# Kernel tuning notes

Measured on AMD Instinct MI355X. Metric: run time of the kernel, lower is better.

Reference implementation:

```python
import jax, jax.numpy as jnp
import numpy as np

N = 50000          # nodes
E = 800000         # edges (avg degree 16)
IN, HID, OUT = 128, 32, 64
H1, H2, H3 = 4, 4, 6
NEG_SLOPE = 0.2


def setup_inputs() -> dict:
    key = jax.random.key(0)
    ks = jax.random.split(key, 18)

    def p(k, shape, fan_in):
        return (jax.random.normal(k, shape, jnp.float32) / np.sqrt(fan_in)).astype(jnp.float32)

    return {
        "x": jax.random.normal(ks[0], (N, IN), jnp.float32),
        "src": jax.random.randint(ks[1], (E,), 0, N, jnp.int32),
        "dst": jax.random.randint(ks[2], (E,), 0, N, jnp.int32),
        # layer 1: IN -> (H1, HID)
        "W1": p(ks[3], (IN, H1 * HID), IN),
        "al1": p(ks[4], (H1, HID), HID),
        "ar1": p(ks[5], (H1, HID), HID),
        "b1": jnp.zeros((H1 * HID,), jnp.float32),
        # layer 2: H1*HID -> (H2, HID), residual (identity since H1*HID == H2*HID... == in)
        "W2": p(ks[6], (H1 * HID, H2 * HID), H1 * HID),
        "al2": p(ks[7], (H2, HID), HID),
        "ar2": p(ks[8], (H2, HID), HID),
        "b2": jnp.zeros((H2 * HID,), jnp.float32),
        # layer 3: H2*HID -> (H3, OUT), residual via linear projection
        "W3": p(ks[9], (H2 * HID, H3 * OUT), H2 * HID),
        "al3": p(ks[10], (H3, OUT), OUT),
        "ar3": p(ks[11], (H3, OUT), OUT),
        "b3": jnp.zeros((H3 * OUT,), jnp.float32),
        "Wres3": p(ks[12], (H2 * HID, H3 * OUT), H2 * HID),
    }


def _gat_layer(h, W, al, ar, b, src, dst, H, D, resval=None):
    # DGL GATConv: proj, per-edge attention logits, leaky-relu, edge softmax
    # over destination neighborhoods, weighted gather-scatter aggregation.
    feat = (h @ W).reshape(N, H, D)                     # [N,H,D]
    el = jnp.sum(feat * al, axis=-1)                    # [N,H]
    er = jnp.sum(feat * ar, axis=-1)                    # [N,H]
    e = jax.nn.leaky_relu(el[src] + er[dst], NEG_SLOPE) # [E,H]
    # numerically-stable segment softmax over dst
    m = jax.ops.segment_max(e, dst, num_segments=N)     # [N,H]
    ex = jnp.exp(e - m[dst])
    s = jax.ops.segment_sum(ex, dst, num_segments=N)    # [N,H]
    a = ex / s[dst]                                     # [E,H]
    msg = feat[src] * a[..., None]                      # [E,H,D]
    rst = jax.ops.segment_sum(msg, dst, num_segments=N) # [N,H,D]
    if resval is not None:
        rst = rst + resval
    return rst + b.reshape(1, H, D)


def reference(x, src, dst, W1, al1, ar1, b1, W2, al2, ar2, b2,
              W3, al3, ar3, b3, Wres3):
    h = jax.nn.elu(_gat_layer(x, W1, al1, ar1, b1, src, dst, H1, HID))
    h = h.reshape(N, H1 * HID)
    h2 = jax.nn.elu(_gat_layer(h, W2, al2, ar2, b2, src, dst, H2, HID,
                               resval=h.reshape(N, H2, HID)))
    h2 = h2.reshape(N, H2 * HID)
    h3 = _gat_layer(h2, W3, al3, ar3, b3, src, dst, H3, OUT,
                    resval=(h2 @ Wres3).reshape(N, H3, OUT))
    return h3.mean(axis=1)                              # [N,OUT]
```

## Files before the change

### kernel.cpp

```cpp
#include <hip/hip_runtime.h>
#include <hip/hip_bf16.h>


#define NODES 50000
#define EDGES 800000
#define NEG 0.2f

typedef __attribute__((ext_vector_type(8))) short bh8;
typedef __attribute__((ext_vector_type(4))) float f4;

__device__ __forceinline__ float leaky(float e) { return e > 0.f ? e : NEG * e; }
__device__ __forceinline__ float blo(unsigned u) { return __uint_as_float(u << 16); }
__device__ __forceinline__ float bhi(unsigned u) { return __uint_as_float(u & 0xffff0000u); }
__device__ __forceinline__ unsigned f2bf(float f) {
    unsigned u = __float_as_uint(f);
    return (u + 0x7fffu + ((u >> 16) & 1u)) >> 16;
}
__device__ __forceinline__ void bfsplit(float z, unsigned& hi, unsigned& lo) {
    hi = f2bf(z);
    float rem = z - __uint_as_float(hi << 16);
    lo = f2bf(rem);
}

#define SW(row, bc) (((row) << 8) + ((bc) ^ (((row) & 7) << 4)))

__global__ void k_cast(const float* __restrict__ in, unsigned short* __restrict__ outb, int n4) {
    int gid = blockIdx.x * blockDim.x + threadIdx.x;
    if (gid >= n4) return;
    float4 v = *reinterpret_cast<const float4*>(in + (size_t)gid * 4);
    unsigned u0 = f2bf(v.x) | (f2bf(v.y) << 16);
    unsigned u1 = f2bf(v.z) | (f2bf(v.w) << 16);
    *reinterpret_cast<uint2*>(outb + (size_t)gid * 4) = make_uint2(u0, u1);
}

__global__ void k_prepw(const float* __restrict__ W, unsigned short* __restrict__ WT, int F) {
    int gid = blockIdx.x * blockDim.x + threadIdx.x;
    if (gid >= 128 * F) return;
    int k = gid / F, f = gid - k * F;
    WT[(size_t)f * 128 + k] = (unsigned short)f2bf(W[gid]);
}

__global__ void k_prep_bt2(const float* __restrict__ W3, const float* __restrict__ Wres3,
                           unsigned short* __restrict__ BT2) {
    int gid = blockIdx.x * blockDim.x + threadIdx.x;
    if (gid >= 64 * 896) return;
    int d = gid / 896, k = gid - d * 896;
    float v;
    if (k < 768) {
        v = W3[(size_t)(k & 127) * 384 + (k >> 7) * 64 + d];
    } else {
        int kr = k - 768;
        v = 0.f;
#pragma unroll
        for (int h = 0; h < 6; ++h) v += Wres3[(size_t)kr * 384 + h * 64 + d];
    }
    BT2[(size_t)d * 896 + k] = (unsigned short)f2bf(v);
}

__global__ void k_prep_alr3(const float* __restrict__ W3, const float* __restrict__ al3,
                            const float* __restrict__ ar3, float* __restrict__ al3c,
                            float* __restrict__ ar3c) {
    int gid = blockIdx.x * blockDim.x + threadIdx.x;
    if (gid >= 1536) return;
    int g = (gid < 768) ? gid : gid - 768;
    int h = g >> 7, k = g & 127;
    const float* a = (gid < 768) ? al3 : ar3;
    float s = 0.f;
#pragma unroll
    for (int d = 0; d < 64; ++d) s += W3[(size_t)k * 384 + h * 64 + d] * a[h * 64 + d];
    if (gid < 768) al3c[g] = s; else ar3c[g] = s;
}

__global__ void k_prep_mb(const float* __restrict__ b3, float* __restrict__ mb) {
    int d = threadIdx.x;
    if (d >= 64) return;
    float s = 0.f;
#pragma unroll
    for (int h = 0; h < 6; ++h) s += b3[h * 64 + d];
    mb[d] = s * (1.f / 6.f);
}

__global__ void k_hist(const int* __restrict__ dst, int* __restrict__ cnt, int e) {
    int gid = blockIdx.x * blockDim.x + threadIdx.x;
    if (gid < e) atomicAdd(&cnt[dst[gid]], 1);
}

__global__ void k_bsum(const int* __restrict__ deg, int* __restrict__ bsum, int n) {
    __shared__ int sm[256];
    int t = threadIdx.x;
    int i = blockIdx.x * 256 + t;
    sm[t] = (i < n) ? deg[i] : 0;
    __syncthreads();
#pragma unroll
    for (int off = 128; off > 0; off >>= 1) {
        if (t < off) sm[t] += sm[t + off];
        __syncthreads();
    }
    if (t == 0) bsum[blockIdx.x] = sm[0];
}

__global__ void k_bscan(const int* __restrict__ bsum, int* __restrict__ bpre, int nb) {
    __shared__ int sm[256];
    int t = threadIdx.x;
    int v = (t < nb) ? bsum[t] : 0;
    sm[t] = v;
    __syncthreads();
    for (int off = 1; off < 256; off <<= 1) {
        int u = (t >= off) ? sm[t - off] : 0;
        __syncthreads();
        sm[t] += u;
        __syncthreads();
    }
    if (t < nb) bpre[t] = sm[t] - v;
}

__global__ void k_offs(const int* __restrict__ deg, const int* __restrict__ bpre,
                       int* __restrict__ offs, int n, int e) {
    __shared__ int sm[256];
    int t = threadIdx.x;
    int i = blockIdx.x * 256 + t;
    int v = (i < n) ? deg[i] : 0;
    sm[t] = v;
    __syncthreads();
    for (int off = 1; off < 256; off <<= 1) {
        int u = (t >= off) ? sm[t - off] : 0;
        __syncthreads();
        sm[t] += u;
        __syncthreads();
    }
    if (i < n) offs[i] = bpre[blockIdx.x] + sm[t] - v;
    if (i == 0) offs[n] = e;
}

__global__ void k_fill(const int* __restrict__ src, const int* __restrict__ dst,
                       const int* __restrict__ offs, int* __restrict__ cur,
                       int* __restrict__ csr, int* __restrict__ nid, int e) {
    int gid = blockIdx.x * blockDim.x + threadIdx.x;
    if (gid < e) {
        int d = dst[gid];
        int pos = offs[d] + atomicAdd(&cur[d], 1);
        csr[pos] = src[gid];
        nid[pos] = d;
    }
}

__global__ void k_ew4(const int* __restrict__ csr, const int* __restrict__ nid,
                      const float* __restrict__ el, const float* __restrict__ er,
                      unsigned short* __restrict__ aw, int e) {
    int gid = blockIdx.x * blockDim.x + threadIdx.x;
    if (gid >= e) return;
    int s = csr[gid], d = nid[gid];
    float4 l4 = *reinterpret_cast<const float4*>(el + (size_t)s * 4);
    float4 r4 = *reinterpret_cast<const float4*>(er + (size_t)d * 4);
    float w0 = __expf(leaky(l4.x + r4.x));
    float w1 = __expf(leaky(l4.y + r4.y));
    float w2 = __expf(leaky(l4.z + r4.z));
    float w3 = __expf(leaky(l4.w + r4.w));
    unsigned u0 = f2bf(w0) | (f2bf(w1) << 16);
    unsigned u1 = f2bf(w2) | (f2bf(w3) << 16);
    *reinterpret_cast<uint2*>(aw + (size_t)gid * 4) = make_uint2(u0, u1);
}

__global__ void k_ew6(const int* __restrict__ csr, const int* __restrict__ nid,
                      const float* __restrict__ el, const float* __restrict__ er,
                      unsigned short* __restrict__ aw, int e) {
    int gid = blockIdx.x * blockDim.x + threadIdx.x;
    if (gid >= e) return;
    int s = csr[gid], d = nid[gid];
    const float2* lp = reinterpret_cast<const float2*>(el + (size_t)s * 6);
    const float2* rp = reinterpret_cast<const float2*>(er + (size_t)d * 6);
    float2 l0 = lp[0], l1 = lp[1], l2 = lp[2];
    float2 r0 = rp[0], r1 = rp[1], r2 = rp[2];
    unsigned w01 = f2bf(__expf(leaky(l0.x + r0.x))) | (f2bf(__expf(leaky(l0.y + r0.y))) << 16);
    unsigned w23 = f2bf(__expf(leaky(l1.x + r1.x))) | (f2bf(__expf(leaky(l1.y + r1.y))) << 16);
    unsigned w45 = f2bf(__expf(leaky(l2.x + r2.x))) | (f2bf(__expf(leaky(l2.y + r2.y))) << 16);
    unsigned char* wb = reinterpret_cast<unsigned char*>(aw) + (size_t)gid * 12;
    *reinterpret_cast<unsigned*>(wb + 0) = w01;
    *reinterpret_cast<unsigned*>(wb + 4) = w23;
    *reinterpret_cast<unsigned*>(wb + 8) = w45;
}

__global__ __launch_bounds__(256) void k_mgemm128(const unsigned short* __restrict__ A,
                                                  const unsigned short* __restrict__ BT,
                                                  unsigned short* __restrict__ C0,
                                                  int nrows) {
    __shared__ char Alds[64 * 256];
    __shared__ char Blds[64 * 256];
    const int t  = threadIdx.x;
    const int n0 = blockIdx.x * 64;
    const int w  = t >> 6;
    const int l  = t & 63;
    const int lr = l & 15;
    const int lk = l >> 4;

    {
        int col8 = (t & 15) * 8;
        int bc   = col8 * 2;
#pragma unroll
        for (int p = 0; p < 4; ++p) {
            int row = p * 16 + (t >> 4);
            int gr  = n0 + row;
            uint4 v = make_uint4(0, 0, 0, 0);
            if (gr < nrows) v = *reinterpret_cast<const uint4*>(A + (size_t)gr * 128 + col8);
            *reinterpret_cast<uint4*>(Alds + SW(row, bc)) = v;
        }
    }

    const int rbase = (w & 1) * 32;
    const int cbase = (w >> 1) * 32;

    for (int ct = 0; ct < 2; ++ct) {
        __syncthreads();
        {
            int col8 = (t & 15) * 8;
            int bc   = col8 * 2;
#pragma unroll
            for (int p = 0; p < 4; ++p) {
                int row = p * 16 + (t >> 4);
                uint4 v = *reinterpret_cast<const uint4*>(BT + (size_t)(ct * 64 + row) * 128 + col8);
                *reinterpret_cast<uint4*>(Blds + SW(row, bc)) = v;
            }
        }
        __syncthreads();

        f4 acc00 = {0.f, 0.f, 0.f, 0.f}, acc01 = {0.f, 0.f, 0.f, 0.f};
        f4 acc10 = {0.f, 0.f, 0.f, 0.f}, acc11 = {0.f, 0.f, 0.f, 0.f};
#pragma unroll
        for (int kk = 0; kk < 4; ++kk) {
            int bck = kk * 64 + lk * 16;
            bh8 a0 = *reinterpret_cast<const bh8*>(Alds + SW(rbase + lr, bck));
            bh8 a1 = *reinterpret_cast<const bh8*>(Alds + SW(rbase + 16 + lr, bck));
            bh8 b0 = *reinterpret_cast<const bh8*>(Blds + SW(cbase + lr, bck));
            bh8 b1 = *reinterpret_cast<const bh8*>(Blds + SW(cbase + 16 + lr, bck));
            acc00 = __builtin_amdgcn_mfma_f32_16x16x32_bf16(a0, b0, acc00, 0, 0, 0);
            acc01 = __builtin_amdgcn_mfma_f32_16x16x32_bf16(a0, b1, acc01, 0, 0, 0);
            acc10 = __builtin_amdgcn_mfma_f32_16x16x32_bf16(a1, b0, acc10, 0, 0, 0);
            acc11 = __builtin_amdgcn_mfma_f32_16x16x32_bf16(a1, b1, acc11, 0, 0, 0);
        }

        const f4* accs[4] = {&acc00, &acc01, &acc10, &acc11};
#pragma unroll
        for (int m = 0; m < 2; ++m) {
#pragma unroll
            for (int j = 0; j < 4; ++j) {
                int gr = n0 + rbase + m * 16 + lk * 4 + j;
                if (gr >= nrows) continue;
#pragma unroll
                for (int n = 0; n < 2; ++n) {
                    float v = (*accs[m * 2 + n])[j];
                    C0[(size_t)gr * 128 + ct * 64 + cbase + n * 16 + lr] = (unsigned short)f2bf(v);
                }
            }
        }
    }
}

__global__ __launch_bounds__(256) void k_mtail2(const unsigned short* __restrict__ zb,
                                                const unsigned short* __restrict__ z2b,
                                                const unsigned short* __restrict__ h2b,
                                                const unsigned short* __restrict__ BT2,
                                                const float* __restrict__ mb,
                                                float* __restrict__ out, int nrows) {
    __shared__ char Alds[128 * 256];
    __shared__ char Blds[64 * 256];
    const int t  = threadIdx.x;
    const int n0 = blockIdx.x * 128;
    const int w  = t >> 6;
    const int l  = t & 63;
    const int lr = l & 15;
    const int lk = l >> 4;
    const int rbase = w * 32;

    f4 acc00 = {0,0,0,0}, acc01 = {0,0,0,0}, acc02 = {0,0,0,0}, acc03 = {0,0,0,0};
    f4 acc10 = {0,0,0,0}, acc11 = {0,0,0,0}, acc12 = {0,0,0,0}, acc13 = {0,0,0,0};

    for (int kt = 0; kt < 13; ++kt) {
        const int bkt = (kt < 6) ? kt : (kt < 12 ? kt - 6 : 6);
        __syncthreads();
        {
            int col8 = (t & 15) * 8;
            int bc   = col8 * 2;
            int rr   = t >> 4;
#pragma unroll
            for (int p = 0; p < 8; ++p) {
                int row = p * 16 + rr;
                int gr  = n0 + row;
                uint4 v = make_uint4(0, 0, 0, 0);
                if (gr < nrows) {
                    const unsigned short* ap =
                        (kt < 6)  ? zb  + (size_t)gr * 768 + kt * 128 :
                        (kt < 12) ? z2b + (size_t)gr * 768 + (kt - 6) * 128 :
                                    h2b + (size_t)gr * 128;
                    v = *reinterpret_cast<const uint4*>(ap + col8);
                }
                *reinterpret_cast<uint4*>(Alds + SW(row, bc)) = v;
            }
#pragma unroll
            for (int p = 0; p < 4; ++p) {
                int row = p * 16 + rr;
                uint4 v = *reinterpret_cast<const uint4*>(BT2 + (size_t)row * 896 + bkt * 128 + col8);
                *reinterpret_cast<uint4*>(Blds + SW(row, bc)) = v;
            }
        }
        __syncthreads();
#pragma unroll
        for (int kk = 0; kk < 4; ++kk) {
            int bck = kk * 64 + lk * 16;
            bh8 a0 = *reinterpret_cast<const bh8*>(Alds + SW(rbase + lr, bck));
            bh8 a1 = *reinterpret_cast<const bh8*>(Alds + SW(rbase + 16 + lr, bck));
            bh8 b0 = *reinterpret_cast<const bh8*>(Blds + SW(0 * 16 + lr, bck));
            bh8 b1 = *reinterpret_cast<const bh8*>(Blds + SW(1 * 16 + lr, bck));
            bh8 b2 = *reinterpret_cast<const bh8*>(Blds + SW(2 * 16 + lr, bck));
            bh8 b3 = *reinterpret_cast<const bh8*>(Blds + SW(3 * 16 + lr, bck));
            acc00 = __builtin_amdgcn_mfma_f32_16x16x32_bf16(a0, b0, acc00, 0, 0, 0);
            acc01 = __builtin_amdgcn_mfma_f32_16x16x32_bf16(a0, b1, acc01, 0, 0, 0);
            acc02 = __builtin_amdgcn_mfma_f32_16x16x32_bf16(a0, b2, acc02, 0, 0, 0);
            acc03 = __builtin_amdgcn_mfma_f32_16x16x32_bf16(a0, b3, acc03, 0, 0, 0);
            acc10 = __builtin_amdgcn_mfma_f32_16x16x32_bf16(a1, b0, acc10, 0, 0, 0);
            acc11 = __builtin_amdgcn_mfma_f32_16x16x32_bf16(a1, b1, acc11, 0, 0, 0);
            acc12 = __builtin_amdgcn_mfma_f32_16x16x32_bf16(a1, b2, acc12, 0, 0, 0);
            acc13 = __builtin_amdgcn_mfma_f32_16x16x32_bf16(a1, b3, acc13, 0, 0, 0);
        }
    }

    const f4* accs[2][4] = {{&acc00, &acc01, &acc02, &acc03},
                            {&acc10, &acc11, &acc12, &acc13}};
#pragma unroll
    for (int m = 0; m < 2; ++m) {
#pragma unroll
        for (int j = 0; j < 4; ++j) {
            int gr = n0 + rbase + m * 16 + lk * 4 + j;
            if (gr >= nrows) continue;
#pragma unroll
            for (int n = 0; n < 4; ++n) {
                int col = n * 16 + lr;
                float v = (*accs[m][n])[j];
                out[(size_t)gr * 64 + col] = v * (1.f / 6.f) + mb[col];
            }
        }
    }
}

template <int H, int D>
__global__ void k_elr_bf(const unsigned short* __restrict__ feat,
                         const float* __restrict__ al, const float* __restrict__ ar,
                         float* __restrict__ el, float* __restrict__ er, int total) {
    int gid = blockIdx.x * blockDim.x + threadIdx.x;
    if (gid >= total) return;
    int n = gid / H, h = gid - n * H;
    const uint4* f = reinterpret_cast<const uint4*>(feat + (size_t)n * (H * D) + h * D);
    const float4* a = reinterpret_cast<const float4*>(al + h * D);
    const float4* r = reinterpret_cast<const float4*>(ar + h * D);
    float sl = 0.f, sr = 0.f;
#pragma unroll
    for (int j = 0; j < D / 8; ++j) {
        uint4 v = f[j];
        float4 a0 = a[2 * j], a1 = a[2 * j + 1];
        float4 r0 = r[2 * j], r1 = r[2 * j + 1];
        float x0 = blo(v.x), x1 = bhi(v.x), x2 = blo(v.y), x3 = bhi(v.y);
        float x4 = blo(v.z), x5 = bhi(v.z), x6 = blo(v.w), x7 = bhi(v.w);
        sl += x0 * a0.x + x1 * a0.y + x2 * a0.z + x3 * a0.w +
              x4 * a1.x + x5 * a1.y + x6 * a1.z + x7 * a1.w;
        sr += x0 * r0.x + x1 * r0.y + x2 * r0.z + x3 * r0.w +
              x4 * r1.x + x5 * r1.y + x6 * r1.z + x7 * r1.w;
    }
    el[gid] = sl;
    er[gid] = sr;
}

__global__ void k_elr3(const unsigned short* __restrict__ h2b,
                       const float* __restrict__ al3c, const float* __restrict__ ar3c,
                       float* __restrict__ el, float* __restrict__ er, int total) {
    int gid = blockIdx.x * blockDim.x + threadIdx.x;
    if (gid >= total) return;
    int n = gid / 6, h = gid - n * 6;
    const uint4* f = reinterpret_cast<const uint4*>(h2b + (size_t)n * 128);
    const float4* a = reinterpret_cast<const float4*>(al3c + h * 128);
    const float4* r = reinterpret_cast<const float4*>(ar3c + h * 128);
    float sl = 0.f, sr = 0.f;
#pragma unroll
    for (int j = 0; j < 16; ++j) {
        uint4 v = f[j];
        float4 a0 = a[2 * j], a1 = a[2 * j + 1];
        float4 r0 = r[2 * j], r1 = r[2 * j + 1];
        float x0 = blo(v.x), x1 = bhi(v.x), x2 = blo(v.y), x3 = bhi(v.y);
        float x4 = blo(v.z), x5 = bhi(v.z), x6 = blo(v.w), x7 = bhi(v.w);
        sl += x0 * a0.x + x1 * a0.y + x2 * a0.z + x3 * a0.w +
              x4 * a1.x + x5 * a1.y + x6 * a1.z + x7 * a1.w;
        sr += x0 * r0.x + x1 * r0.y + x2 * r0.z + x3 * r0.w +
              x4 * r1.x + x5 * r1.y + x6 * r1.z + x7 * r1.w;
    }
    el[gid] = sl;
    er[gid] = sr;
}

template <bool HASRES, bool WRITEF32>
__global__ __launch_bounds__(256) void k_aggr128c(
    const unsigned short* __restrict__ feat, const int* __restrict__ csr,
    const int* __restrict__ offs, const unsigned short* __restrict__ aw,
    const float* __restrict__ bias, const float* __restrict__ resf,
    unsigned short* __restrict__ outb, float* __restrict__ outf, int nnodes) {
    int node = blockIdx.x * 4 + (threadIdx.x >> 6);
    if (node >= nnodes) return;
    int l = threadIdx.x & 63;
    int half = l >> 5;
    int ll = l & 31;
    int h = ll >> 3;
    int o0 = offs[node], o1 = offs[node + 1];
    float acc0 = 0.f, acc1 = 0.f, acc2 = 0.f, acc3 = 0.f, s = 0.f;
    int nt = (o1 - o0 + 1) >> 1;
#pragma unroll 2
    for (int t = 0; t < nt; ++t) {
        int ei = o0 + 2 * t + half;
        bool v = ei < o1;
        int pos = v ? ei : o0;
        uint2 wu = *reinterpret_cast<const uint2*>(aw + (size_t)pos * 4);
        unsigned uw = (h & 2) ? wu.y : wu.x;
        float w = (h & 1) ? bhi(uw) : blo(uw);
        w = v ? w : 0.f;
        s += w;
        int sidx = csr[pos];
        uint2 u = *reinterpret_cast<const uint2*>(feat + (size_t)sidx * 128 + 4 * ll);
        acc0 = fmaf(w, blo(u.x), acc0);
        acc1 = fmaf(w, bhi(u.x), acc1);
        acc2 = fmaf(w, blo(u.y), acc2);
        acc3 = fmaf(w, bhi(u.y), acc3);
    }
    s    += __shfl_xor(s, 32);
    acc0 += __shfl_xor(acc0, 32);
    acc1 += __shfl_xor(acc1, 32);
    acc2 += __shfl_xor(acc2, 32);
    acc3 += __shfl_xor(acc3, 32);
    float inv = (o1 > o0) ? 1.f / s : 0.f;
    int f = 4 * ll;
    float4 bi = *reinterpret_cast<const float4*>(bias + f);
    float r0 = acc0 * inv + bi.x;
    float r1 = acc1 * inv + bi.y;
    float r2 = acc2 * inv + bi.z;
    float r3 = acc3 * inv + bi.w;
    if (HASRES) {
        float4 rv = *reinterpret_cast<const float4*>(resf + (size_t)node * 128 + f);
        r0 += rv.x; r1 += rv.y; r2 += rv.z; r3 += rv.w;
    }
    r0 = (r0 > 0.f) ? r0 : (__expf(r0) - 1.f);
    r1 = (r1 > 0.f) ? r1 : (__expf(r1) - 1.f);
    r2 = (r2 > 0.f) ? r2 : (__expf(r2) - 1.f);
    r3 = (r3 > 0.f) ? r3 : (__expf(r3) - 1.f);
    if (half == 0) {
        unsigned u0 = f2bf(r0) | (f2bf(r1) << 16);
        unsigned u1 = f2bf(r2) | (f2bf(r3) << 16);
        *reinterpret_cast<uint2*>(outb + (size_t)node * 128 + f) = make_uint2(u0, u1);
        if (WRITEF32)
            *reinterpret_cast<float4*>(outf + (size_t)node * 128 + f) =
                make_float4(r0, r1, r2, r3);
    }
}

__global__ __launch_bounds__(256) void k_aggrZ2(
    const unsigned short* __restrict__ h2b, const int* __restrict__ csr,
    const int* __restrict__ offs, const unsigned short* __restrict__ aw6,
    unsigned short* __restrict__ zb, unsigned short* __restrict__ z2b, int nnodes) {
    int node = blockIdx.x * 4 + (threadIdx.x >> 6);
    if (node >= nnodes) return;
    int l = threadIdx.x & 63;
    int half = l >> 5;
    int ll = l & 31;
    float acc[6][4];
    float s[6];
#pragma unroll
    for (int h = 0; h < 6; ++h) {
        s[h] = 0.f;
#pragma unroll
        for (int j = 0; j < 4; ++j) acc[h][j] = 0.f;
    }
    int o0 = offs[node], o1 = offs[node + 1];
    int nt = (o1 - o0 + 1) >> 1;
    const unsigned char* awb = reinterpret_cast<const unsigned char*>(aw6);
#pragma unroll 2
    for (int t = 0; t < nt; ++t) {
        int ei = o0 + 2 * t + half;
        bool v = ei < o1;
        int pos = v ? ei : o0;
        const unsigned char* wb = awb + (size_t)pos * 12;
        unsigned w01 = *reinterpret_cast<const unsigned*>(wb + 0);
        unsigned w23 = *reinterpret_cast<const unsigned*>(wb + 4);
        unsigned w45 = *reinterpret_cast<const unsigned*>(wb + 8);
        float wv[6] = {blo(w01), bhi(w01), blo(w23), bhi(w23), blo(w45), bhi(w45)};
        int sidx = csr[pos];
        uint2 u = *reinterpret_cast<const uint2*>(h2b + (size_t)sidx * 128 + 4 * ll);
        float f0 = blo(u.x), f1 = bhi(u.x), f2 = blo(u.y), f3 = bhi(u.y);
#pragma unroll
        for (int h = 0; h < 6; ++h) {
            float w = v ? wv[h] : 0.f;
            s[h] += w;
            acc[h][0] = fmaf(w, f0, acc[h][0]);
            acc[h][1] = fmaf(w, f1, acc[h][1]);
            acc[h][2] = fmaf(w, f2, acc[h][2]);
            acc[h][3] = fmaf(w, f3, acc[h][3]);
        }
    }
    bool has = o1 > o0;
#pragma unroll
    for (int h = 0; h < 6; ++h) {
        s[h] += __shfl_xor(s[h], 32);
#pragma unroll
        for (int j = 0; j < 4; ++j) acc[h][j] += __shfl_xor(acc[h][j], 32);
    }
    if (half == 0) {
#pragma unroll
        for (int h = 0; h < 6; ++h) {
            float inv = has ? 1.f / s[h] : 0.f;
            unsigned hi0, lo0, hi1, lo1, hi2, lo2, hi3, lo3;
            bfsplit(acc[h][0] * inv, hi0, lo0);
            bfsplit(acc[h][1] * inv, hi1, lo1);
            bfsplit(acc[h][2] * inv, hi2, lo2);
            bfsplit(acc[h][3] * inv, hi3, lo3);
            size_t off = (size_t)node * 768 + h * 128 + 4 * ll;
            *reinterpret_cast<uint2*>(zb + off)  = make_uint2(hi0 | (hi1 << 16), hi2 | (hi3 << 16));
            *reinterpret_cast<uint2*>(z2b + off) = make_uint2(lo0 | (lo1 << 16), lo2 | (lo3 << 16));
        }
    }
}

extern "C" void kernel_launch(void* const* d_in, const int* in_sizes, int n_in,
                              void* d_out, int out_size, void* d_ws, size_t ws_size,
                              hipStream_t stream) {
    const float* x     = (const float*)d_in[0];
    const int*   src   = (const int*)d_in[1];
    const int*   dst   = (const int*)d_in[2];
    const float* W1    = (const float*)d_in[3];
    const float* al1   = (const float*)d_in[4];
    const float* ar1   = (const float*)d_in[5];
    const float* b1    = (const float*)d_in[6];
    const float* W2    = (const float*)d_in[7];
    const float* al2   = (const float*)d_in[8];
    const float* ar2   = (const float*)d_in[9];
    const float* b2    = (const float*)d_in[10];
    const float* W3    = (const float*)d_in[11];
    const float* al3   = (const float*)d_in[12];
    const float* ar3   = (const float*)d_in[13];
    const float* b3    = (const float*)d_in[14];
    const float* Wres3 = (const float*)d_in[15];
    float* out = (float*)d_out;

    const int N = NODES, E = EDGES;
    const int NB = (N + 255) / 256;

    char*  ws = (char*)d_ws;
    size_t o  = 0;
    auto alloc = [&](size_t bytes) {
        size_t r = o;
        o += (bytes + 255) & ~(size_t)255;
        return r;
    };
    int*            offs  = (int*)(ws + alloc((size_t)(N + 1) * 4));
    int*            cnt   = (int*)(ws + alloc((size_t)N * 4));
    int*            csr   = (int*)(ws + alloc((size_t)E * 4));
    float*          el    = (float*)(ws + alloc((size_t)N * 6 * 4));
    float*          er    = (float*)(ws + alloc((size_t)N * 6 * 4));
    unsigned short* aw    = (unsigned short*)(ws + alloc((size_t)E * 6 * 2));
    unsigned short* h2b   = (unsigned short*)(ws + alloc((size_t)N * 128 * 2));
    unsigned short* w1t   = (unsigned short*)(ws + alloc((size_t)128 * 128 * 2));
    unsigned short* w2t   = (unsigned short*)(ws + alloc((size_t)128 * 128 * 2));
    unsigned short* bt2   = (unsigned short*)(ws + alloc((size_t)64 * 896 * 2));
    float*          al3c  = (float*)(ws + alloc((size_t)768 * 4));
    float*          ar3c  = (float*)(ws + alloc((size_t)768 * 4));
    float*          mb    = (float*)(ws + alloc((size_t)64 * 4));
    int*            bsum  = (int*)(ws + alloc((size_t)256 * 4));
    int*            bpre  = (int*)(ws + alloc((size_t)256 * 4));
    char* U = ws + alloc((size_t)N * 768 * 2 * 2);
    unsigned short* xb    = (unsigned short*)(U);
    unsigned short* featb = (unsigned short*)(U + (size_t)N * 128 * 2);
    unsigned short* h1b   = (unsigned short*)(U + (size_t)N * 256 * 2);
    float*          h1f   = (float*)(U + (size_t)N * 384 * 2);
    unsigned short* zb    = (unsigned short*)(U);
    unsigned short* z2b   = (unsigned short*)(U + (size_t)N * 768 * 2);
    int*            nid   = (int*)(U + (size_t)N * 768 * 2);

    const int gE = (E + 255) / 256;
    const int g4 = (N * 4 + 255) / 256;
    const int g6 = (N * 6 + 255) / 256;
    const int gA = (N + 3) / 4;
    const int gG = (N + 63) / 64;
    const int gT = (N + 127) / 128;

    k_cast<<<(N * 128 / 4 + 255) / 256, 256, 0, stream>>>(x, xb, N * 128 / 4);
    k_prepw<<<(128 * 128 + 255) / 256, 256, 0, stream>>>(W1, w1t, 128);
    k_prepw<<<(128 * 128 + 255) / 256, 256, 0, stream>>>(W2, w2t, 128);
    k_prep_bt2<<<(64 * 896 + 255) / 256, 256, 0, stream>>>(W3, Wres3, bt2);
    k_prep_alr3<<<6, 256, 0, stream>>>(W3, al3, ar3, al3c, ar3c);
    k_prep_mb<<<1, 64, 0, stream>>>(b3, mb);

    hipMemsetAsync(cnt, 0, (size_t)N * 4, stream);
    k_hist<<<gE, 256, 0, stream>>>(dst, cnt, E);
    k_bsum<<<NB, 256, 0, stream>>>(cnt, bsum, N);
    k_bscan<<<1, 256, 0, stream>>>(bsum, bpre, NB);
    k_offs<<<NB, 256, 0, stream>>>(cnt, bpre, offs, N, E);
    hipMemsetAsync(cnt, 0, (size_t)N * 4, stream);
    k_fill<<<gE, 256, 0, stream>>>(src, dst, offs, cnt, csr, nid, E);

    k_mgemm128<<<gG, 256, 0, stream>>>(xb, w1t, featb, N);
    k_elr_bf<4, 32><<<g4, 256, 0, stream>>>(featb, al1, ar1, el, er, N * 4);
    k_ew4<<<gE, 256, 0, stream>>>(csr, nid, el, er, aw, E);
    k_aggr128c<false, true><<<gA, 256, 0, stream>>>(featb, csr, offs, aw, b1,
                                                    nullptr, h1b, h1f, N);

    k_mgemm128<<<gG, 256, 0, stream>>>(h1b, w2t, featb, N);
    k_elr_bf<4, 32><<<g4, 256, 0, stream>>>(featb, al2, ar2, el, er, N * 4);
    k_ew4<<<gE, 256, 0, stream>>>(csr, nid, el, er, aw, E);
    k_aggr128c<true, false><<<gA, 256, 0, stream>>>(featb, csr, offs, aw, b2,
                                                    h1f, h2b, nullptr, N);

    k_elr3<<<g6, 256, 0, stream>>>(h2b, al3c, ar3c, el, er, N * 6);
    k_ew6<<<gE, 256, 0, stream>>>(csr, nid, el, er, aw, E);
    k_aggrZ2<<<gA, 256, 0, stream>>>(h2b, csr, offs, aw, zb, z2b, N);
    k_mtail2<<<gT, 256, 0, stream>>>(zb, z2b, h2b, bt2, mb, out, N);
}
```

Baseline: 433.0 us.

## Precompute softmax denominators and move bf16 hi/lo split into tail GEMM

Adds separate per-node kernels that sum the edge attention weights and store reciprocal denominators, so the aggregation kernels no longer carry per-head sums, validity masking and shuffles. Invalid edges now point at a zero-filled sentinel slot instead of being masked. Layer 3 aggregation writes fp32 z directly, and the tail GEMM splits it into bf16 hi/lo inside LDS and issues extra MFMAs for the low part. This replaces two bf16 arrays with one fp32 array of the same size. The cost is three extra kernel launches, another pass over the edge weights, and more LDS in the tail GEMM, which may lower its occupancy.

```diff
diff --git a/kernel.cpp b/kernel.cpp
--- a/kernel.cpp
+++ b/kernel.cpp
@@ -16,10 +16,12 @@
     unsigned u = __float_as_uint(f);
     return (u + 0x7fffu + ((u >> 16) & 1u)) >> 16;
 }
-__device__ __forceinline__ void bfsplit(float z, unsigned& hi, unsigned& lo) {
-    hi = f2bf(z);
-    float rem = z - __uint_as_float(hi << 16);
-    lo = f2bf(rem);
+__device__ __forceinline__ void pk2(float a, float b, unsigned& hi, unsigned& lo) {
+    unsigned ha = f2bf(a), hb = f2bf(b);
+    float ra = a - __uint_as_float(ha << 16);
+    float rb = b - __uint_as_float(hb << 16);
+    hi = ha | (hb << 16);
+    lo = f2bf(ra) | (f2bf(rb) << 16);
 }
 
 #define SW(row, bc) (((row) << 8) + ((bc) ^ (((row) & 7) << 4)))
@@ -180,6 +182,44 @@
     *reinterpret_cast<unsigned*>(wb + 8) = w45;
 }
 
+__global__ void k_denom4(const unsigned short* __restrict__ aw,
+                         const int* __restrict__ offs, float* __restrict__ inv4, int n) {
+    int gid = blockIdx.x * blockDim.x + threadIdx.x;
+    if (gid >= n) return;
+    int o0 = offs[gid], o1 = offs[gid + 1];
+    float s0 = 0.f, s1 = 0.f, s2 = 0.f, s3 = 0.f;
+    for (int p = o0; p < o1; ++p) {
+        uint2 wu = *reinterpret_cast<const uint2*>(aw + (size_t)p * 4);
+        s0 += blo(wu.x); s1 += bhi(wu.x);
+        s2 += blo(wu.y); s3 += bhi(wu.y);
+    }
+    float4 r = (o1 > o0) ? make_float4(1.f / s0, 1.f / s1, 1.f / s2, 1.f / s3)
+                         : make_float4(0.f, 0.f, 0.f, 0.f);
+    *reinterpret_cast<float4*>(inv4 + (size_t)gid * 4) = r;
+}
+
+__global__ void k_denom6(const unsigned short* __restrict__ aw,
+                         const int* __restrict__ offs, float* __restrict__ inv6, int n) {
+    int gid = blockIdx.x * blockDim.x + threadIdx.x;
+    if (gid >= n) return;
+    int o0 = offs[gid], o1 = offs[gid + 1];
+    float s[6] = {0.f, 0.f, 0.f, 0.f, 0.f, 0.f};
+    const unsigned char* awb = reinterpret_cast<const unsigned char*>(aw);
+    for (int p = o0; p < o1; ++p) {
+        const unsigned char* wb = awb + (size_t)p * 12;
+        unsigned w01 = *reinterpret_cast<const unsigned*>(wb + 0);
+        unsigned w23 = *reinterpret_cast<const unsigned*>(wb + 4);
+        unsigned w45 = *reinterpret_cast<const unsigned*>(wb + 8);
+        s[0] += blo(w01); s[1] += bhi(w01);
+        s[2] += blo(w23); s[3] += bhi(w23);
+        s[4] += blo(w45); s[5] += bhi(w45);
+    }
+    bool has = o1 > o0;
+    float* o = inv6 + (size_t)gid * 6;
+#pragma unroll
+    for (int h = 0; h < 6; ++h) o[h] = has ? 1.f / s[h] : 0.f;
+}
+
 __global__ __launch_bounds__(256) void k_mgemm128(const unsigned short* __restrict__ A,
                                                   const unsigned short* __restrict__ BT,
                                                   unsigned short* __restrict__ C0,
@@ -255,13 +295,13 @@
     }
 }
 
-__global__ __launch_bounds__(256) void k_mtail2(const unsigned short* __restrict__ zb,
-                                                const unsigned short* __restrict__ z2b,
+__global__ __launch_bounds__(256) void k_mtail3(const float* __restrict__ zf,
                                                 const unsigned short* __restrict__ h2b,
                                                 const unsigned short* __restrict__ BT2,
                                                 const float* __restrict__ mb,
                                                 float* __restrict__ out, int nrows) {
-    __shared__ char Alds[128 * 256];
+    __shared__ char Ahi[128 * 256];
+    __shared__ char Alo[128 * 256];
     __shared__ char Blds[64 * 256];
     const int t  = threadIdx.x;
     const int n0 = blockIdx.x * 128;
@@ -274,8 +314,7 @@
     f4 acc00 = {0,0,0,0}, acc01 = {0,0,0,0}, acc02 = {0,0,0,0}, acc03 = {0,0,0,0};
     f4 acc10 = {0,0,0,0}, acc11 = {0,0,0,0}, acc12 = {0,0,0,0}, acc13 = {0,0,0,0};
 
-    for (int kt = 0; kt < 13; ++kt) {
-        const int bkt = (kt < 6) ? kt : (kt < 12 ? kt - 6 : 6);
+    for (int kt = 0; kt < 7; ++kt) {
         __syncthreads();
         {
             int col8 = (t & 15) * 8;
@@ -285,20 +324,32 @@
             for (int p = 0; p < 8; ++p) {
                 int row = p * 16 + rr;
                 int gr  = n0 + row;
-                uint4 v = make_uint4(0, 0, 0, 0);
-                if (gr < nrows) {
-                    const unsigned short* ap =
-                        (kt < 6)  ? zb  + (size_t)gr * 768 + kt * 128 :
-                        (kt < 12) ? z2b + (size_t)gr * 768 + (kt - 6) * 128 :
-                                    h2b + (size_t)gr * 128;
-                    v = *reinterpret_cast<const uint4*>(ap + col8);
+                if (kt < 6) {
+                    float4 v0 = make_float4(0.f, 0.f, 0.f, 0.f);
+                    float4 v1 = make_float4(0.f, 0.f, 0.f, 0.f);
+                    if (gr < nrows) {
+                        const float* ap = zf + (size_t)gr * 768 + kt * 128 + col8;
+                        v0 = *reinterpret_cast<const float4*>(ap);
+                        v1 = *reinterpret_cast<const float4*>(ap + 4);
+                    }
+                    unsigned h0, l0, h1, l1, h2_, l2_, h3, l3;
+                    pk2(v0.x, v0.y, h0, l0);
+                    pk2(v0.z, v0.w, h1, l1);
+                    pk2(v1.x, v1.y, h2_, l2_);
+                    pk2(v1.z, v1.w, h3, l3);
+                    *reinterpret_cast<uint4*>(Ahi + SW(row, bc)) = make_uint4(h0, h1, h2_, h3);
+                    *reinterpret_cast<uint4*>(Alo + SW(row, bc)) = make_uint4(l0, l1, l2_, l3);
+                } else {
+                    uint4 v = make_uint4(0, 0, 0, 0);
+                    if (gr < nrows)
+                        v = *reinterpret_cast<const uint4*>(h2b + (size_t)gr * 128 + col8);
+                    *reinterpret_cast<uint4*>(Ahi + SW(row, bc)) = v;
                 }
-                *reinterpret_cast<uint4*>(Alds + SW(row, bc)) = v;
             }
 #pragma unroll
             for (int p = 0; p < 4; ++p) {
                 int row = p * 16 + rr;
-                uint4 v = *reinterpret_cast<const uint4*>(BT2 + (size_t)row * 896 + bkt * 128 + col8);
+                uint4 v = *reinterpret_cast<const uint4*>(BT2 + (size_t)row * 896 + kt * 128 + col8);
                 *reinterpret_cast<uint4*>(Blds + SW(row, bc)) = v;
             }
         }
@@ -306,12 +357,12 @@
 #pragma unroll
         for (int kk = 0; kk < 4; ++kk) {
             int bck = kk * 64 + lk * 16;
-            bh8 a0 = *reinterpret_cast<const bh8*>(Alds + SW(rbase + lr, bck));
-            bh8 a1 = *reinterpret_cast<const bh8*>(Alds + SW(rbase + 16 + lr, bck));
             bh8 b0 = *reinterpret_cast<const bh8*>(Blds + SW(0 * 16 + lr, bck));
             bh8 b1 = *reinterpret_cast<const bh8*>(Blds + SW(1 * 16 + lr, bck));
             bh8 b2 = *reinterpret_cast<const bh8*>(Blds + SW(2 * 16 + lr, bck));
             bh8 b3 = *reinterpret_cast<const bh8*>(Blds + SW(3 * 16 + lr, bck));
+            bh8 a0 = *reinterpret_cast<const bh8*>(Ahi + SW(rbase + lr, bck));
+            bh8 a1 = *reinterpret_cast<const bh8*>(Ahi + SW(rbase + 16 + lr, bck));
             acc00 = __builtin_amdgcn_mfma_f32_16x16x32_bf16(a0, b0, acc00, 0, 0, 0);
             acc01 = __builtin_amdgcn_mfma_f32_16x16x32_bf16(a0, b1, acc01, 0, 0, 0);
             acc02 = __builtin_amdgcn_mfma_f32_16x16x32_bf16(a0, b2, acc02, 0, 0, 0);
@@ -320,6 +371,18 @@
             acc11 = __builtin_amdgcn_mfma_f32_16x16x32_bf16(a1, b1, acc11, 0, 0, 0);
             acc12 = __builtin_amdgcn_mfma_f32_16x16x32_bf16(a1, b2, acc12, 0, 0, 0);
             acc13 = __builtin_amdgcn_mfma_f32_16x16x32_bf16(a1, b3, acc13, 0, 0, 0);
+            if (kt < 6) {
+                bh8 c0 = *reinterpret_cast<const bh8*>(Alo + SW(rbase + lr, bck));
+                bh8 c1 = *reinterpret_cast<const bh8*>(Alo + SW(rbase + 16 + lr, bck));
+                acc00 = __builtin_amdgcn_mfma_f32_16x16x32_bf16(c0, b0, acc00, 0, 0, 0);
+                acc01 = __builtin_amdgcn_mfma_f32_16x16x32_bf16(c0, b1, acc01, 0, 0, 0);
+                acc02 = __builtin_amdgcn_mfma_f32_16x16x32_bf16(c0, b2, acc02, 0, 0, 0);
+                acc03 = __builtin_amdgcn_mfma_f32_16x16x32_bf16(c0, b3, acc03, 0, 0, 0);
+                acc10 = __builtin_amdgcn_mfma_f32_16x16x32_bf16(c1, b0, acc10, 0, 0, 0);
+                acc11 = __builtin_amdgcn_mfma_f32_16x16x32_bf16(c1, b1, acc11, 0, 0, 0);
+                acc12 = __builtin_amdgcn_mfma_f32_16x16x32_bf16(c1, b2, acc12, 0, 0, 0);
+                acc13 = __builtin_amdgcn_mfma_f32_16x16x32_bf16(c1, b3, acc13, 0, 0, 0);
+            }
         }
     }
 
@@ -395,11 +458,12 @@
 }
 
 template <bool HASRES, bool WRITEF32>
-__global__ __launch_bounds__(256) void k_aggr128c(
+__global__ __launch_bounds__(256) void k_aggr128d(
     const unsigned short* __restrict__ feat, const int* __restrict__ csr,
     const int* __restrict__ offs, const unsigned short* __restrict__ aw,
-    const float* __restrict__ bias, const float* __restrict__ resf,
-    unsigned short* __restrict__ outb, float* __restrict__ outf, int nnodes) {
+    const float* __restrict__ inv4, const float* __restrict__ bias,
+    const float* __restrict__ resf, unsigned short* __restrict__ outb,
+    float* __restrict__ outf, int nnodes) {
     int node = blockIdx.x * 4 + (threadIdx.x >> 6);
     if (node >= nnodes) return;
     int l = threadIdx.x & 63;
@@ -407,18 +471,15 @@
     int ll = l & 31;
     int h = ll >> 3;
     int o0 = offs[node], o1 = offs[node + 1];
-    float acc0 = 0.f, acc1 = 0.f, acc2 = 0.f, acc3 = 0.f, s = 0.f;
+    float acc0 = 0.f, acc1 = 0.f, acc2 = 0.f, acc3 = 0.f;
     int nt = (o1 - o0 + 1) >> 1;
 #pragma unroll 2
     for (int t = 0; t < nt; ++t) {
         int ei = o0 + 2 * t + half;
-        bool v = ei < o1;
-        int pos = v ? ei : o0;
+        int pos = (ei < o1) ? ei : EDGES;
         uint2 wu = *reinterpret_cast<const uint2*>(aw + (size_t)pos * 4);
         unsigned uw = (h & 2) ? wu.y : wu.x;
         float w = (h & 1) ? bhi(uw) : blo(uw);
-        w = v ? w : 0.f;
-        s += w;
         int sidx = csr[pos];
         uint2 u = *reinterpret_cast<const uint2*>(feat + (size_t)sidx * 128 + 4 * ll);
         acc0 = fmaf(w, blo(u.x), acc0);
@@ -426,12 +487,11 @@
         acc2 = fmaf(w, blo(u.y), acc2);
         acc3 = fmaf(w, bhi(u.y), acc3);
     }
-    s    += __shfl_xor(s, 32);
     acc0 += __shfl_xor(acc0, 32);
     acc1 += __shfl_xor(acc1, 32);
     acc2 += __shfl_xor(acc2, 32);
     acc3 += __shfl_xor(acc3, 32);
-    float inv = (o1 > o0) ? 1.f / s : 0.f;
+    float inv = inv4[(size_t)node * 4 + h];
     int f = 4 * ll;
     float4 bi = *reinterpret_cast<const float4*>(bias + f);
     float r0 = acc0 * inv + bi.x;
@@ -456,31 +516,27 @@
     }
 }
 
-__global__ __launch_bounds__(256) void k_aggrZ2(
+__global__ __launch_bounds__(256) void k_aggrZ3(
     const unsigned short* __restrict__ h2b, const int* __restrict__ csr,
     const int* __restrict__ offs, const unsigned short* __restrict__ aw6,
-    unsigned short* __restrict__ zb, unsigned short* __restrict__ z2b, int nnodes) {
+    const float* __restrict__ inv6, float* __restrict__ zf, int nnodes) {
     int node = blockIdx.x * 4 + (threadIdx.x >> 6);
     if (node >= nnodes) return;
     int l = threadIdx.x & 63;
     int half = l >> 5;
     int ll = l & 31;
     float acc[6][4];
-    float s[6];
-#pragma unroll
-    for (int h = 0; h < 6; ++h) {
-        s[h] = 0.f;
+#pragma unroll
+    for (int h = 0; h < 6; ++h)
 #pragma unroll
         for (int j = 0; j < 4; ++j) acc[h][j] = 0.f;
-    }
     int o0 = offs[node], o1 = offs[node + 1];
     int nt = (o1 - o0 + 1) >> 1;
     const unsigned char* awb = reinterpret_cast<const unsigned char*>(aw6);
 #pragma unroll 2
     for (int t = 0; t < nt; ++t) {
         int ei = o0 + 2 * t + half;
-        bool v = ei < o1;
-        int pos = v ? ei : o0;
+        int pos = (ei < o1) ? ei : EDGES;
         const unsigned char* wb = awb + (size_t)pos * 12;
         unsigned w01 = *reinterpret_cast<const unsigned*>(wb + 0);
         unsigned w23 = *reinterpret_cast<const unsigned*>(wb + 4);
@@ -491,33 +547,26 @@
         float f0 = blo(u.x), f1 = bhi(u.x), f2 = blo(u.y), f3 = bhi(u.y);
 #pragma unroll
         for (int h = 0; h < 6; ++h) {
-            float w = v ? wv[h] : 0.f;
-            s[h] += w;
-            acc[h][0] = fmaf(w, f0, acc[h][0]);
-            acc[h][1] = fmaf(w, f1, acc[h][1]);
-            acc[h][2] = fmaf(w, f2, acc[h][2]);
-            acc[h][3] = fmaf(w, f3, acc[h][3]);
-        }
-    }
-    bool has = o1 > o0;
-#pragma unroll
-    for (int h = 0; h < 6; ++h) {
-        s[h] += __shfl_xor(s[h], 32);
+            acc[h][0] = fmaf(wv[h], f0, acc[h][0]);
+            acc[h][1] = fmaf(wv[h], f1, acc[h][1]);
+            acc[h][2] = fmaf(wv[h], f2, acc[h][2]);
+            acc[h][3] = fmaf(wv[h], f3, acc[h][3]);
+        }
+    }
+#pragma unroll
+    for (int h = 0; h < 6; ++h)
 #pragma unroll
         for (int j = 0; j < 4; ++j) acc[h][j] += __shfl_xor(acc[h][j], 32);
-    }
     if (half == 0) {
+        float2 i01 = *reinterpret_cast<const float2*>(inv6 + (size_t)node * 6 + 0);
+        float2 i23 = *reinterpret_cast<const float2*>(inv6 + (size_t)node * 6 + 2);
+        float2 i45 = *reinterpret_cast<const float2*>(inv6 + (size_t)node * 6 + 4);
+        float iv[6] = {i01.x, i01.y, i23.x, i23.y, i45.x, i45.y};
 #pragma unroll
         for (int h = 0; h < 6; ++h) {
-            float inv = has ? 1.f / s[h] : 0.f;
-            unsigned hi0, lo0, hi1, lo1, hi2, lo2, hi3, lo3;
-            bfsplit(acc[h][0] * inv, hi0, lo0);
-            bfsplit(acc[h][1] * inv, hi1, lo1);
-            bfsplit(acc[h][2] * inv, hi2, lo2);
-            bfsplit(acc[h][3] * inv, hi3, lo3);
-            size_t off = (size_t)node * 768 + h * 128 + 4 * ll;
-            *reinterpret_cast<uint2*>(zb + off)  = make_uint2(hi0 | (hi1 << 16), hi2 | (hi3 << 16));
-            *reinterpret_cast<uint2*>(z2b + off) = make_uint2(lo0 | (lo1 << 16), lo2 | (lo3 << 16));
+            *reinterpret_cast<float4*>(zf + (size_t)node * 768 + h * 128 + 4 * ll) =
+                make_float4(acc[h][0] * iv[h], acc[h][1] * iv[h],
+                            acc[h][2] * iv[h], acc[h][3] * iv[h]);
         }
     }
 }
@@ -555,10 +604,11 @@
     };
     int*            offs  = (int*)(ws + alloc((size_t)(N + 1) * 4));
     int*            cnt   = (int*)(ws + alloc((size_t)N * 4));
-    int*            csr   = (int*)(ws + alloc((size_t)E * 4));
+    int*            csr   = (int*)(ws + alloc((size_t)(E + 1) * 4));
     float*          el    = (float*)(ws + alloc((size_t)N * 6 * 4));
     float*          er    = (float*)(ws + alloc((size_t)N * 6 * 4));
-    unsigned short* aw    = (unsigned short*)(ws + alloc((size_t)E * 6 * 2));
+    unsigned short* aw    = (unsigned short*)(ws + alloc((size_t)(E + 1) * 6 * 2));
+    float*          inv   = (float*)(ws + alloc((size_t)N * 6 * 4));
     unsigned short* h2b   = (unsigned short*)(ws + alloc((size_t)N * 128 * 2));
     unsigned short* w1t   = (unsigned short*)(ws + alloc((size_t)128 * 128 * 2));
     unsigned short* w2t   = (unsigned short*)(ws + alloc((size_t)128 * 128 * 2));
@@ -568,18 +618,18 @@
     float*          mb    = (float*)(ws + alloc((size_t)64 * 4));
     int*            bsum  = (int*)(ws + alloc((size_t)256 * 4));
     int*            bpre  = (int*)(ws + alloc((size_t)256 * 4));
-    char* U = ws + alloc((size_t)N * 768 * 2 * 2);
+    char* U = ws + alloc((size_t)N * 768 * 4);
     unsigned short* xb    = (unsigned short*)(U);
     unsigned short* featb = (unsigned short*)(U + (size_t)N * 128 * 2);
     unsigned short* h1b   = (unsigned short*)(U + (size_t)N * 256 * 2);
     float*          h1f   = (float*)(U + (size_t)N * 384 * 2);
-    unsigned short* zb    = (unsigned short*)(U);
-    unsigned short* z2b   = (unsigned short*)(U + (size_t)N * 768 * 2);
-    int*            nid   = (int*)(U + (size_t)N * 768 * 2);
+    int*            nid   = (int*)(U + (size_t)64 * 1024 * 1024);
+    float*          zf    = (float*)(U);
 
     const int gE = (E + 255) / 256;
     const int g4 = (N * 4 + 255) / 256;
     const int g6 = (N * 6 + 255) / 256;
+    const int gN = (N + 255) / 256;
     const int gA = (N + 3) / 4;
     const int gG = (N + 63) / 64;
     const int gT = (N + 127) / 128;
@@ -590,6 +640,10 @@
     k_prep_bt2<<<(64 * 896 + 255) / 256, 256, 0, stream>>>(W3, Wres3, bt2);
     k_prep_alr3<<<6, 256, 0, stream>>>(W3, al3, ar3, al3c, ar3c);
     k_prep_mb<<<1, 64, 0, stream>>>(b3, mb);
+
+    hipMemsetAsync(csr + E, 0, 4, stream);
+    hipMemsetAsync((char*)aw + (size_t)E * 8, 0, 8, stream);
+    hipMemsetAsync((char*)aw + (size_t)E * 12, 0, 12, stream);
 
     hipMemsetAsync(cnt, 0, (size_t)N * 4, stream);
     k_hist<<<gE, 256, 0, stream>>>(dst, cnt, E);
@@ -602,17 +656,20 @@
     k_mgemm128<<<gG, 256, 0, stream>>>(xb, w1t, featb, N);
     k_elr_bf<4, 32><<<g4, 256, 0, stream>>>(featb, al1, ar1, el, er, N * 4);
     k_ew4<<<gE, 256, 0, stream>>>(csr, nid, el, er, aw, E);
-    k_aggr128c<false, true><<<gA, 256, 0, stream>>>(featb, csr, offs, aw, b1,
+    k_denom4<<<gN, 256, 0, stream>>>(aw, offs, inv, N);
+    k_aggr128d<false, true><<<gA, 256, 0, stream>>>(featb, csr, offs, aw, inv, b1,
                                                     nullptr, h1b, h1f, N);
 
     k_mgemm128<<<gG, 256, 0, stream>>>(h1b, w2t, featb, N);
     k_elr_bf<4, 32><<<g4, 256, 0, stream>>>(featb, al2, ar2, el, er, N * 4);
     k_ew4<<<gE, 256, 0, stream>>>(csr, nid, el, er, aw, E);
-    k_aggr128c<true, false><<<gA, 256, 0, stream>>>(featb, csr, offs, aw, b2,
+    k_denom4<<<gN, 256, 0, stream>>>(aw, offs, inv, N);
+    k_aggr128d<true, false><<<gA, 256, 0, stream>>>(featb, csr, offs, aw, inv, b2,
                                                     h1f, h2b, nullptr, N);
 
     k_elr3<<<g6, 256, 0, stream>>>(h2b, al3c, ar3c, el, er, N * 6);
     k_ew6<<<gE, 256, 0, stream>>>(csr, nid, el, er, aw, E);
-    k_aggrZ2<<<gA, 256, 0, stream>>>(h2b, csr, offs, aw, zb, z2b, N);
-    k_mtail2<<<gT, 256, 0, stream>>>(zb, z2b, h2b, bt2, mb, out, N);
-}
+    k_denom6<<<gN, 256, 0, stream>>>(aw, offs, inv, N);
+    k_aggrZ3<<<gA, 256, 0, stream>>>(h2b, csr, offs, aw, inv, zf, N);
+    k_mtail3<<<gT, 256, 0, stream>>>(zf, h2b, bt2, mb, out, N);
+}
```

Measured after the change: 444.8 us. 2.7% more time.
